# Kernel optimization log

Measured on AMD Instinct MI355X. Metric: run time of the kernel, lower is better.

Reference implementation:

```python
import jax, jax.numpy as jnp
import numpy as np

B = 1024          # sub (= obj) batch size
NUME = 20000      # num entities
NUMR = 8          # num relations
NET = 2 * NUMR + 1  # hetero edge types: r, -r, self
DIMT = 28         # time encoding dim
DIME = 100        # entity embedding dim
DIM = 200         # emb module output dim
H = 4             # history length
HEADS = 4         # GAT heads
OH = DIM // HEADS # GAT per-head out dim
N0 = 160000       # layer-0 src nodes
N1 = 40000        # layer-0 dst / layer-1 src nodes
R = 2 * B * H     # unique roots = layer-1 dst nodes
E0 = 60000        # edges per etype, layer 0
E1 = 16000        # edges per etype, layer 1
K = 500000        # copy mask entries
DIMR = 100        # relation embedding dim
HATT = 4          # self-attention heads
OA = DIM // HATT  # per-head q/k/v dim (Attention out_dim//h)
DIN0 = DIME + DIMT
DIN1 = DIM + DIMT


def setup_inputs() -> dict:
    key = jax.random.key(0)
    ks = jax.random.split(key, 48)
    ri = jax.random.randint
    nrm = lambda i, shp, s=0.05: jax.random.normal(ks[i], shp, jnp.float32) * s
    d = {}
    d['sub'] = ri(ks[0], (B,), 0, NUME)
    d['obj'] = ri(ks[1], (B,), 0, NUME)
    d['rel'] = ri(ks[2], (B,), 0, NUMR)
    d['ts'] = 1000
    d['nid0'] = ri(ks[3], (N0,), 0, NUME * 1000)
    d['root_idx'] = ri(ks[4], (2 * B * H,), 0, R)
    d['src0'] = ri(ks[5], (NET, E0), 0, N0)
    d['dst0'] = ri(ks[6], (NET, E0), 0, N1)
    d['src1'] = ri(ks[7], (NET, E1), 0, N1)
    d['dst1'] = ri(ks[8], (NET, E1), 0, R)
    d['copy_rows'] = ri(ks[9], (K,), 0, 2 * B)
    d['copy_cols'] = ri(ks[10], (K,), 0, NUME)
    # parameters
    d['emb_table'] = nrm(11, (NUME, DIME))
    d['time_freq'] = jnp.asarray(1.0 / 10 ** np.linspace(0, 9, DIMT), jnp.float32)
    d['time_phase'] = jnp.zeros((DIMT,), jnp.float32)
    d['Wg0'] = nrm(12, (NET, DIN0, HEADS, OH))
    d['al0'] = nrm(13, (NET, HEADS, OH))
    d['ar0'] = nrm(14, (NET, HEADS, OH))
    d['bg0'] = jnp.zeros((NET, DIM), jnp.float32)
    d['Wg1'] = nrm(15, (NET, DIN1, HEADS, OH))
    d['al1'] = nrm(16, (NET, HEADS, OH))
    d['ar1'] = nrm(17, (NET, HEADS, OH))
    d['bg1'] = jnp.zeros((NET, DIM), jnp.float32)
    d['ln0_w'] = jnp.ones((H * DIM,), jnp.float32)
    d['ln0_b'] = jnp.zeros((H * DIM,), jnp.float32)
    d['Wq'] = nrm(18, (HATT, DIM, OA))
    d['bq'] = jnp.zeros((HATT, OA), jnp.float32)
    d['Wv'] = nrm(19, (HATT, DIM, OA))
    d['bv'] = jnp.zeros((HATT, OA), jnp.float32)
    d['ln1_w'] = jnp.ones((H * DIM,), jnp.float32)
    d['ln1_b'] = jnp.zeros((H * DIM,), jnp.float32)
    d['Wd1'] = nrm(20, (H * DIM, DIM))
    d['bd1'] = jnp.zeros((DIM,), jnp.float32)
    d['srel_emb'] = nrm(21, (NUMR, DIMR))
    d['orel_emb'] = nrm(22, (NUMR, DIMR))
    d['Wsub'] = nrm(23, (DIM + DIMR, NUME))
    d['bsub'] = jnp.zeros((NUME,), jnp.float32)
    d['Wobj'] = nrm(24, (DIM + DIMR, NUME))
    d['bobj'] = jnp.zeros((NUME,), jnp.float32)
    d['csrel_emb'] = nrm(25, (NUMR, DIMR))
    d['corel_emb'] = nrm(26, (NUMR, DIMR))
    d['cWsub'] = nrm(27, (DIM + DIMR, NUME))
    d['cbsub'] = jnp.zeros((NUME,), jnp.float32)
    d['cWobj'] = nrm(28, (DIM + DIMR, NUME))
    d['cbobj'] = jnp.zeros((NUME,), jnp.float32)
    return d


def _temb(nid, ts, tf, tp):
    t = (ts - nid // NUME).astype(jnp.float32)
    return jnp.cos(t[:, None] * tf + tp)


def _gat(x, Wg, al, ar, bg, src, dst, nd):
    # heterogeneous GATConv over NET relation types, mean-aggregated (DGL HeteroGraphConv)
    msg = jnp.zeros((nd, HEADS, OH), x.dtype)
    for r in range(NET):
        s, d = src[r], dst[r]
        fs = jnp.einsum('ei,iho->eho', x[s], Wg[r])                     # [E,h,o] src feats per edge
        er_n = (jnp.einsum('ni,iho->nho', x[:nd], Wg[r]) * ar[r]).sum(-1)  # [nd,h]
        el = (fs * al[r]).sum(-1)                                       # [E,h]
        e = jax.nn.leaky_relu(el + er_n[d], 0.2)
        m = jax.ops.segment_max(e, d, num_segments=nd)
        a = jnp.exp(e - m[d])
        z = jax.ops.segment_sum(a, d, num_segments=nd)
        alpha = a / z[d]
        msg = msg + jax.ops.segment_sum(alpha[:, :, None] * fs, d, num_segments=nd)
    return jax.nn.relu((msg.reshape(nd, HEADS * OH) + bg.sum(0)) / NET)


def _ln(x, w, b):
    mu = x.mean(-1, keepdims=True)
    v = ((x - mu) ** 2).mean(-1, keepdims=True)
    return (x - mu) / jnp.sqrt(v + 1e-5) * w + b


def reference(sub, obj, rel, ts, nid0, root_idx, src0, dst0, src1, dst1, copy_rows, copy_cols, emb_table, time_freq, time_phase, Wg0, al0, ar0, bg0, Wg1, al1, ar1, bg1, ln0_w, ln0_b, Wq, bq, Wv, bv, ln1_w, ln1_b, Wd1, bd1, srel_emb, orel_emb, Wsub, bsub, Wobj, bobj, csrel_emb, corel_emb, cWsub, cbsub, cWobj, cbobj):
    # --- EmbModule: entity emb + time enc + 2-layer hetero GAT over sampled blocks ---
    h = emb_table[nid0 % NUME]                                   # [N0, DIME]
    x = jnp.concatenate([h, _temb(nid0, ts, time_freq, time_phase)], 1)
    h = _gat(x, Wg0, al0, ar0, bg0, src0, dst0, N1)              # [N1, DIM]
    x = jnp.concatenate([h, _temb(nid0[:N1], ts, time_freq, time_phase)], 1)
    h = _gat(x, Wg1, al1, ar1, bg1, src1, dst1, R)               # [R, DIM]
    hid = h[root_idx].reshape(2 * B, H * DIM)                    # [2B, H*DIM]
    # --- Copy mechanism (on detached last-history embedding) ---
    ch = jax.lax.stop_gradient(hid[:, -DIM:])
    raw_sub = jnp.concatenate([ch[B:], corel_emb[rel]], 1) @ cWsub + cbsub
    raw_obj = jnp.concatenate([ch[:B], csrel_emb[rel]], 1) @ cWobj + cbobj
    raw = jnp.concatenate([raw_sub, raw_obj], 0)                 # [2B, NUME]
    masked = jnp.full((2 * B, NUME), -100.0, raw.dtype).at[copy_rows, copy_cols].set(raw[copy_rows, copy_cols])
    csub, cobj = masked[:B], masked[B:]
    # --- Gen layers: LN -> SelfAttention -> LN -> dense ---
    x = _ln(hid, ln0_w, ln0_b)
    xs = x.reshape(2 * B, H, DIM)
    q = jnp.einsum('bse,heo->bhso', xs, Wq) + bq[:, None, :]     # k == q (w_q reused in source)
    att = jax.nn.softmax(jnp.einsum('bhso,bhto->bhst', q, q), axis=2)  # torch softmax(dim=1)
    v = jnp.einsum('bse,heo->bhso', xs, Wv) + bv[:, None, :]
    ans = jnp.einsum('bhst,bhto->bhso', att, v)                  # [2B,h,S,OA]
    x = jax.nn.relu(ans.transpose(0, 2, 1, 3).reshape(2 * B, H * DIM))
    x = _ln(x, ln1_w, ln1_b)
    x = jax.nn.relu(x @ Wd1 + bd1)                               # [2B, DIM]
    sub_emb, obj_emb = x[:B], x[B:]
    sub_pred = jnp.concatenate([obj_emb, orel_emb[rel]], 1) @ Wsub + bsub
    obj_pred = jnp.concatenate([sub_emb, srel_emb[rel]], 1) @ Wobj + bobj
    return (sub_pred, obj_pred, csub, cobj)
```

## Files before the change

kernel.cpp:

```cpp
#include <hip/hip_runtime.h>
#include <hip/hip_bf16.h>
#include <math.h>

typedef __hip_bfloat16 bf16;
typedef __attribute__((ext_vector_type(8))) short short8;
typedef __attribute__((ext_vector_type(4))) float f32x4;

#define BQ 1024
#define NUME 20000
#define NET 17
#define DIMT 28
#define DIME 100
#define DIM 200
#define HEADS 4
#define OH 50
#define N0 160000
#define N1 40000
#define RNODES 8192
#define E0 60000
#define E1 16000
#define KK 500000
#define DIMR 100
#define HATT 4
#define OA 50
#define DIN0 128
#define DIN1 228
#define HD 800
#define NROWS 2048
#define PKS 10
#define PNT 1250

__device__ __forceinline__ float b2f(bf16 v){ return __bfloat162float(v); }
__device__ __forceinline__ bf16 f2b(float v){ return __float2bfloat16(v); }
__device__ __forceinline__ float bs2f(unsigned short u){ return __uint_as_float((unsigned)u << 16); }
__device__ __forceinline__ unsigned short f2bu(float v){ bf16 t = f2b(v); return *reinterpret_cast<unsigned short*>(&t); }

static constexpr int CVT_NREG = 29;
static constexpr int CVT_N[CVT_NREG] = {
  2000000, 28, 28, 435200, 3400, 3400, 3400, 775200, 3400, 3400, 3400,
  800, 800, 40000, 200, 40000, 200, 800, 800, 160000, 200, 800, 800,
  20000, 20000, 800, 800, 20000, 20000
};
static constexpr int CVT_DIN[CVT_NREG] = {
  12,13,14,15,16,17,18,19,20,21,22,23,24,25,26,27,28,29,30,31,32,33,34,36,38,39,40,42,44
};
struct CvtSrcs { const void* p[CVT_NREG]; };
struct CvtMeta { int cum[CVT_NREG+1]; int bcum[CVT_NREG+1]; };

__global__ __launch_bounds__(64) void k_detect(const unsigned* tfw, unsigned* flag){
  if (threadIdx.x == 0) flag[0] = ((tfw[0] & 0xFFFFu) == 0u) ? 1u : 0u;
}

__global__ __launch_bounds__(256) void k_cvt(CvtSrcs srcs, CvtMeta meta, bf16* dst, const unsigned* flagp){
  int b = blockIdx.x;
  int r = 0;
  while (meta.bcum[r+1] <= b) r++;
  int i = (b - meta.bcum[r])*256 + threadIdx.x;
  int n = meta.cum[r+1] - meta.cum[r];
  if (i >= n) return;
  bool f32m = flagp[0] != 0u;
  bf16 v;
  if (f32m) v = f2b(((const float*)srcs.p[r])[i]);
  else      v = ((const bf16*)srcs.p[r])[i];
  dst[meta.cum[r] + i] = v;
}

__global__ __launch_bounds__(256) void k_fill_u32(unsigned* p, unsigned v, long n){
  long i = (long)blockIdx.x*256 + threadIdx.x;
  if (i < n) p[i] = v;
}

__global__ __launch_bounds__(256) void k_fill_out(void* outb, const unsigned* flagp){
  bool f32m = flagp[0] != 0u;
  long nwords = f32m ? (long)2*BQ*NUME : (long)BQ*NUME;
  long i = (long)blockIdx.x*256 + threadIdx.x;
  if (i >= nwords) return;
  unsigned* p = (unsigned*)((char*)outb + (size_t)2*BQ*NUME * (f32m ? 4 : 2));
  p[i] = f32m ? 0xC2C80000u : 0xC2C8C2C8u;
}

__global__ __launch_bounds__(256) void k_prep_w(const bf16* Wg, const bf16* al, const bf16* ar,
                                                float* wal, float* war, int DIN){
  int idx = blockIdx.x*256 + threadIdx.x;
  int total = NET*DIN*4;
  if (idx >= total) return;
  int h = idx & 3; int ri = idx >> 2; int i = ri % DIN; int r = ri / DIN;
  const bf16* wrow = Wg + ((size_t)(r*DIN + i))*HEADS*OH + h*OH;
  const bf16* alr = al + (size_t)(r*HEADS + h)*OH;
  const bf16* arr = ar + (size_t)(r*HEADS + h)*OH;
  float sl=0.f, sr=0.f;
  for (int o=0;o<OH;o++){ float w=b2f(wrow[o]); sl += w*b2f(alr[o]); sr += w*b2f(arr[o]); }
  wal[idx]=sl; war[idx]=sr;
}

__global__ __launch_bounds__(256) void k_pack(const bf16* Wg, bf16* wpk, int DIN, int KS){
  int idx = blockIdx.x*256 + threadIdx.x;
  int total = NET*KS*13*512;
  if (idx >= total) return;
  int j = idx & 7, lane = (idx>>3) & 63;
  int rem = idx >> 9;
  int nt = rem % 13, rks = rem / 13;
  int ks = rks % KS, r = rks / KS;
  int k = ks*32 + (lane>>4)*8 + j;
  int n = nt*16 + (lane&15);
  bf16 v = f2b(0.f);
  if (k < DIN && n < 200) v = Wg[((size_t)r*DIN + k)*200 + n];
  wpk[idx] = v;
}

__global__ __launch_bounds__(256) void k_pack_pred(const void* Wsub, const void* Wobj, bf16* wpkP,
                                                    const unsigned* flagp){
  long idx = (long)blockIdx.x*256 + threadIdx.x;
  long total = (long)2*PKS*PNT*512;
  if (idx >= total) return;
  int j = (int)(idx & 7), lane = (int)((idx>>3) & 63);
  long rem = idx >> 9;
  int ntile = (int)(rem % PNT); rem /= PNT;
  int ks = (int)(rem % PKS); int page = (int)(rem / PKS);
  int k = ks*32 + (lane>>4)*8 + j;
  int n = ntile*16 + (lane&15);
  const void* W = page ? Wobj : Wsub;
  bool f32m = flagp[0] != 0u;
  float v = 0.f;
  if (k < 300) v = f32m ? ((const float*)W)[(size_t)k*NUME + n]
                        : b2f(((const bf16*)W)[(size_t)k*NUME + n]);
  wpkP[idx] = f2b(v);
}

__global__ __launch_bounds__(256) void k_prep_pred(const float* x4, const bf16* nSrel, const bf16* nOrel,
                                                    const int* rel, bf16* Apack){
  long idx = (long)blockIdx.x*256 + threadIdx.x;
  if (idx >= (long)2*1024*320) return;
  int j = (int)(idx % 320); long rem = idx/320;
  int row = (int)(rem % 1024); int page = (int)(rem / 1024);
  float v = 0.f;
  if (j < 200) v = x4[((size_t)(page==0 ? 1024+row : row))*DIM + j];
  else if (j < 300){
    const bf16* re = (page==0) ? nOrel : nSrel;
    v = b2f(re[(size_t)rel[row]*DIMR + (j-200)]);
  }
  Apack[idx] = f2b(v);
}

__global__ __launch_bounds__(256) void k_pred_mfma(const bf16* __restrict__ Apack, const bf16* __restrict__ wpkP,
                                                   const bf16* bsub, const bf16* bobj, void* outb,
                                                   const unsigned* flagp){
  constexpr int SR = 320 + 8;
  __shared__ bf16 As[64*SR];
  int page = blockIdx.z;
  int rb = blockIdx.y*64;
  int cb = blockIdx.x*16;
  int t = threadIdx.x;
  const bf16* Ap = Apack + (size_t)page*1024*320;
  for (int c=t; c<64*80; c+=256){
    int m=c/80, j4=c%80;
    *(uint2*)(As + m*SR + j4*4) = *(const uint2*)(Ap + (size_t)(rb+m)*320 + j4*4);
  }
  __syncthreads();
  int lane = t&63, w = t>>6;
  int n_idx = lane&15, quad = lane>>4;
  const short8* wp8 = (const short8*)(wpkP + (size_t)page*PKS*PNT*512);
  f32x4 acc[4][4];
  #pragma unroll
  for (int i=0;i<4;i++)
    #pragma unroll
    for (int mt=0;mt<4;mt++) acc[i][mt] = (f32x4){0.f,0.f,0.f,0.f};
  short8 bz = {0,0,0,0,0,0,0,0};
  for (int ks=0; ks<PKS; ks++){
    short8 bfr[4];
    #pragma unroll
    for (int i=0;i<4;i++){
      int ntile = cb + w + 4*i;
      bfr[i] = (ntile < PNT) ? wp8[((size_t)ks*PNT + ntile)*64 + lane] : bz;
    }
    short8 afr[4];
    #pragma unroll
    for (int mt=0;mt<4;mt++) afr[mt] = *(const short8*)(As + (size_t)(mt*16 + n_idx)*SR + ks*32 + quad*8);
    #pragma unroll
    for (int i=0;i<4;i++)
      #pragma unroll
      for (int mt=0;mt<4;mt++)
        acc[i][mt] = __builtin_amdgcn_mfma_f32_16x16x32_bf16(afr[mt], bfr[i], acc[i][mt], 0, 0, 0);
  }
  bool f32m = flagp[0] != 0u;
  const bf16* bias = page ? bobj : bsub;
  size_t elem_off = (size_t)page*BQ*NUME;
  for (int i=0;i<4;i++){
    int ntile = cb + w + 4*i;
    if (ntile >= PNT) continue;
    int n = ntile*16 + n_idx;
    float bb = b2f(bias[n]);
    #pragma unroll
    for (int mt=0;mt<4;mt++){
      #pragma unroll
      for (int reg=0;reg<4;reg++){
        int m = rb + mt*16 + quad*4 + reg;
        size_t oi = elem_off + (size_t)m*NUME + n;
        float val = acc[i][mt][reg] + bb;
        if (f32m) ((float*)outb)[oi] = val; else ((bf16*)outb)[oi] = f2b(val);
      }
    }
  }
}

__global__ __launch_bounds__(256) void k_bgs(const bf16* bg0, const bf16* bg1, float* bgs0, float* bgs1){
  int j = blockIdx.x*256 + threadIdx.x;
  if (j < DIM){ float s=0.f; for(int r=0;r<NET;r++) s += b2f(bg0[r*DIM+j]); bgs0[j]=s; }
  else if (j < 2*DIM){ int jj=j-DIM; float s=0.f; for(int r=0;r<NET;r++) s += b2f(bg1[r*DIM+jj]); bgs1[jj]=s; }
}

__global__ __launch_bounds__(256) void k_build_x0(const int* nid0, const int* ts_p, const bf16* emb,
                                                  const bf16* tf, const bf16* tp, bf16* x0){
  long idx = (long)blockIdx.x*256 + threadIdx.x;
  if (idx >= (long)N0*DIN0) return;
  int n = idx / DIN0, j = idx % DIN0;
  int nid = nid0[n];
  bf16 v;
  if (j < DIME) v = emb[(size_t)(nid % NUME)*DIME + j];
  else {
    float t = (float)(ts_p[0] - nid / NUME);
    int jj = j - DIME;
    v = f2b(cosf(t * b2f(tf[jj]) + b2f(tp[jj])));
  }
  x0[idx] = v;
}

__global__ __launch_bounds__(256) void k_build_x1(const int* nid0, const int* ts_p, const float* msg0,
                                                  const float* bgs0, const bf16* tf, const bf16* tp, bf16* x1){
  long idx = (long)blockIdx.x*256 + threadIdx.x;
  if (idx >= (long)N1*DIN1) return;
  int n = idx / DIN1, j = idx % DIN1;
  bf16 v;
  if (j < DIM){
    v = f2b(fmaxf((msg0[(size_t)n*DIM + j] + bgs0[j]) * (1.0f/NET), 0.0f));
  } else {
    int nid = nid0[n];
    float t = (float)(ts_p[0] - nid / NUME);
    int jj = j - DIM;
    v = f2b(cosf(t * b2f(tf[jj]) + b2f(tp[jj])));
  }
  x1[idx] = v;
}

template<int DIN>
__global__ __launch_bounds__(256) void k_er(const bf16* __restrict__ x, const float* __restrict__ war,
                                            bf16* __restrict__ er, int nd){
  int idx = blockIdx.x*256 + threadIdx.x;
  if (idx >= NET*nd) return;
  int r = idx / nd, n = idx % nd;
  const ushort4* xr = (const ushort4*)(x + (size_t)n*DIN);
  const float4* w = (const float4*)(war + (size_t)r*DIN*4);
  float a0=0.f,a1=0.f,a2=0.f,a3=0.f;
  #pragma unroll 4
  for (int i=0;i<DIN/4;i++){
    ushort4 xv = xr[i];
    float x0=bs2f(xv.x), x1=bs2f(xv.y), x2=bs2f(xv.z), x3=bs2f(xv.w);
    float4 w0=w[4*i], w1=w[4*i+1], w2=w[4*i+2], w3=w[4*i+3];
    a0 += x0*w0.x + x1*w1.x + x2*w2.x + x3*w3.x;
    a1 += x0*w0.y + x1*w1.y + x2*w2.y + x3*w3.y;
    a2 += x0*w0.z + x1*w1.z + x2*w2.z + x3*w3.z;
    a3 += x0*w0.w + x1*w1.w + x2*w2.w + x3*w3.w;
  }
  bf16* e = er + (size_t)idx*4;
  e[0]=f2b(a0); e[1]=f2b(a1); e[2]=f2b(a2); e[3]=f2b(a3);
}

template<int DIN>
__global__ __launch_bounds__(256) void k_edge(const bf16* __restrict__ x, const float* __restrict__ wal,
                                              const bf16* __restrict__ er,
                                              const int* __restrict__ src, const int* __restrict__ dst,
                                              bf16* abuf, float* z, int nE, int nd){
  int idx = blockIdx.x*256 + threadIdx.x;
  if (idx >= NET*nE) return;
  int r = idx / nE;
  int s = src[idx], d = dst[idx];
  const ushort4* xr = (const ushort4*)(x + (size_t)s*DIN);
  const float4* w = (const float4*)(wal + (size_t)r*DIN*4);
  float a0=0.f,a1=0.f,a2=0.f,a3=0.f;
  #pragma unroll 4
  for (int i=0;i<DIN/4;i++){
    ushort4 xv = xr[i];
    float x0=bs2f(xv.x), x1=bs2f(xv.y), x2=bs2f(xv.z), x3=bs2f(xv.w);
    float4 w0=w[4*i], w1=w[4*i+1], w2=w[4*i+2], w3=w[4*i+3];
    a0 += x0*w0.x + x1*w1.x + x2*w2.x + x3*w3.x;
    a1 += x0*w0.y + x1*w1.y + x2*w2.y + x3*w3.y;
    a2 += x0*w0.z + x1*w1.z + x2*w2.z + x3*w3.z;
    a3 += x0*w0.w + x1*w1.w + x2*w2.w + x3*w3.w;
  }
  float acc[4] = {a0,a1,a2,a3};
  const bf16* ern = er + ((size_t)r*nd + d)*4;
  float* zp = z + ((size_t)r*nd + d)*4;
  bf16* ao = abuf + (size_t)idx*4;
  #pragma unroll
  for (int h=0;h<4;h++){
    float v = acc[h] + b2f(ern[h]);
    v = v>0.f ? v : 0.2f*v;
    float a = expf(fminf(v, 80.f));
    ao[h] = f2b(a);
    atomicAdd(&zp[h], a);
  }
}

__global__ __launch_bounds__(256) void k_count(const int* __restrict__ dst, long n, unsigned* cnt){
  long i = (long)blockIdx.x*256 + threadIdx.x;
  if (i >= n) return;
  atomicAdd(&cnt[dst[i]], 1u);
}

__global__ __launch_bounds__(256) void k_scan(const unsigned* __restrict__ cnt, unsigned* offs, unsigned* cur, int n){
  __shared__ unsigned part[256];
  __shared__ unsigned tot;
  int t = threadIdx.x;
  int chunk = (n + 255)/256;
  int lo = t*chunk, hi = lo+chunk; if (hi > n) hi = n; if (lo > n) lo = n;
  unsigned s = 0;
  for (int i=lo;i<hi;i++) s += cnt[i];
  part[t] = s;
  __syncthreads();
  if (t==0){
    unsigned r = 0;
    for (int i=0;i<256;i++){ unsigned v = part[i]; part[i] = r; r += v; }
    tot = r;
  }
  __syncthreads();
  unsigned run = part[t];
  for (int i=lo;i<hi;i++){ offs[i]=run; cur[i]=run; run += cnt[i]; }
  if (t==0) offs[n] = tot;
}

__global__ __launch_bounds__(256) void k_fillcsr(const int* __restrict__ dst, long n, unsigned* cur, int* ids){
  long i = (long)blockIdx.x*256 + threadIdx.x;
  if (i >= n) return;
  unsigned pos = atomicAdd(&cur[dst[i]], 1u);
  ids[pos] = (int)i;
}

template<int DIN, int KS>
__global__ __launch_bounds__(256) void k_acc_mfma(const bf16* __restrict__ x, const bf16* __restrict__ wpk,
                                                  const bf16* __restrict__ abuf, const float* __restrict__ z,
                                                  const int* __restrict__ src, const int* __restrict__ dst,
                                                  float* msg, bf16* fbuf, int nE, int nd, int r0, int mode){
  constexpr int KM = KS*32;
  constexpr int SR = KM + 8;
  __shared__ bf16 xs[64*SR];
  __shared__ float alpha_s[64*4];
  __shared__ int sdst[64], ssrc[64];
  int r = r0 + blockIdx.y;
  int eb = blockIdx.x*64;
  int me = min(64, nE - eb);
  int t = threadIdx.x;
  if (t < 64){
    int v_src=0, v_dst=0;
    if (t < me){ v_src = src[(size_t)r*nE + eb + t]; v_dst = dst[(size_t)r*nE + eb + t]; }
    ssrc[t]=v_src; sdst[t]=v_dst;
  }
  __syncthreads();
  {
    int m = t>>2, h = t&3;
    float al = 0.f;
    if (m < me){
      float a = b2f(abuf[((size_t)r*nE + eb + m)*4 + h]);
      float zz = z[((size_t)r*nd + sdst[m])*4 + h];
      al = a / fmaxf(zz, 1e-30f);
    }
    alpha_s[m*4+h] = al;
  }
  constexpr int CH = KM/4;
  for (int c = t; c < 64*CH; c += 256){
    int m = c / CH, j4 = c % CH;
    uint2 v = make_uint2(0u,0u);
    if (m < me && j4*4 < DIN) v = *(const uint2*)(x + (size_t)ssrc[m]*DIN + j4*4);
    *(uint2*)(xs + m*SR + j4*4) = v;
  }
  __syncthreads();

  int lane = t & 63, w = t >> 6;
  int n_idx = lane & 15, quad = lane >> 4;
  const short8* wpk8 = (const short8*)wpk;
  for (int mt=0; mt<4; mt++){
    short8 a[KS];
    const bf16* abase = xs + (size_t)(mt*16 + n_idx)*SR + quad*8;
    #pragma unroll
    for (int ks=0; ks<KS; ks++) a[ks] = *(const short8*)(abase + ks*32);
    int m = mt*16 + n_idx;
    for (int nt=w; nt<13; nt+=4){
      const short8* bp = wpk8 + (((size_t)r*KS)*13 + nt)*64 + lane;
      f32x4 acc = {0.f,0.f,0.f,0.f};
      #pragma unroll
      for (int ks=0; ks<KS; ks++){
        short8 b = bp[(size_t)ks*13*64];
        acc = __builtin_amdgcn_mfma_f32_16x16x32_bf16(b, a[ks], acc, 0, 0, 0);
      }
      int nbase = nt*16 + quad*4;
      if (nbase < 200 && m < me){
        if (mode == 0){
          #pragma unroll
          for (int reg=0; reg<4; reg++){
            int n = nbase + reg;
            int h = n / 50;
            atomicAdd(&msg[(size_t)sdst[m]*200 + n], acc[reg] * alpha_s[m*4+h]);
          }
        } else {
          ushort4 pk;
          { int n=nbase;   pk.x = f2bu(acc[0] * alpha_s[m*4 + n/50]); }
          { int n=nbase+1; pk.y = f2bu(acc[1] * alpha_s[m*4 + n/50]); }
          { int n=nbase+2; pk.z = f2bu(acc[2] * alpha_s[m*4 + n/50]); }
          { int n=nbase+3; pk.w = f2bu(acc[3] * alpha_s[m*4 + n/50]); }
          *(ushort4*)(fbuf + ((size_t)(r - r0)*nE + eb + m)*200 + nbase) = pk;
        }
      }
    }
  }
}

__global__ __launch_bounds__(256) void k_gather(const bf16* __restrict__ F, const unsigned* __restrict__ offs,
                                                const int* __restrict__ ids, float* __restrict__ msg,
                                                int nd, int accum){
  int w = threadIdx.x >> 6, lane = threadIdx.x & 63;
  int d = blockIdx.x*4 + w;
  if (d >= nd) return;
  unsigned k0 = offs[d], k1 = offs[d+1];
  float a0=0.f, a1=0.f, a2=0.f, a3=0.f;
  for (unsigned k=k0; k<k1; k++){
    int id = ids[k];
    if (lane < 50){
      ushort4 v = *(const ushort4*)(F + (size_t)id*200 + lane*4);
      a0 += bs2f(v.x); a1 += bs2f(v.y); a2 += bs2f(v.z); a3 += bs2f(v.w);
    }
  }
  if (lane < 50){
    float4* out = (float4*)(msg + (size_t)d*200 + lane*4);
    if (accum){ float4 p = *out; a0 += p.x; a1 += p.y; a2 += p.z; a3 += p.w; }
    float4 o; o.x=a0; o.y=a1; o.z=a2; o.w=a3;
    *out = o;
  }
}

__global__ __launch_bounds__(256) void k_hid(const float* msg1, const float* bgs1, const int* root_idx, float* hid){
  long idx = (long)blockIdx.x*256 + threadIdx.x;
  if (idx >= (long)NROWS*HD) return;
  int b = idx / HD, c = idx % HD;
  int s = c / DIM, j = c % DIM;
  int n = root_idx[b*4 + s];
  hid[idx] = fmaxf((msg1[(size_t)n*DIM + j] + bgs1[j]) * (1.0f/NET), 0.0f);
}

__global__ __launch_bounds__(256) void k_ln(const float* xin, const bf16* w, const bf16* b, float* xout){
  int row = blockIdx.x;
  const float* xr = xin + (size_t)row*HD;
  __shared__ float red[16];
  __shared__ float mu_s, rs_s;
  float s=0.f, s2=0.f;
  for (int j=threadIdx.x;j<HD;j+=256){ float v=xr[j]; s+=v; s2+=v*v; }
  for (int off=32; off; off>>=1){ s += __shfl_down(s,off); s2 += __shfl_down(s2,off); }
  int lane = threadIdx.x & 63, wid = threadIdx.x >> 6;
  if (lane==0){ red[wid]=s; red[8+wid]=s2; }
  __syncthreads();
  if (threadIdx.x==0){
    float S = red[0]+red[1]+red[2]+red[3];
    float S2 = red[8]+red[9]+red[10]+red[11];
    float mu = S * (1.0f/HD);
    float var = fmaxf(S2 * (1.0f/HD) - mu*mu, 0.f);
    mu_s = mu; rs_s = rsqrtf(var + 1e-5f);
  }
  __syncthreads();
  float mu = mu_s, rs = rs_s;
  for (int j=threadIdx.x;j<HD;j+=256){
    float v = (xr[j]-mu)*rs;
    xout[(size_t)row*HD + j] = v*b2f(w[j]) + b2f(b[j]);
  }
}

__global__ __launch_bounds__(256) void k_att(const float* xln, const bf16* Wq, const bf16* bq,
                                             const bf16* Wv, const bf16* bv, float* x2){
  __shared__ float xs[HD], qs[HD], vs[HD], att_s[64];
  int b = blockIdx.x, t = threadIdx.x;
  for (int j=t;j<HD;j+=256) xs[j] = xln[(size_t)b*HD + j];
  __syncthreads();
  for (int idx=t; idx<HD; idx+=256){
    int ha = idx/200, srow=(idx%200)/50, o=idx%50;
    const float* xr = xs + srow*200;
    const bf16* wq = Wq + (size_t)ha*DIM*OA + o;
    const bf16* wv = Wv + (size_t)ha*DIM*OA + o;
    float q=0.f, v=0.f;
    for (int e=0;e<DIM;e++){ float xv=xr[e]; q += xv*b2f(wq[(size_t)e*OA]); v += xv*b2f(wv[(size_t)e*OA]); }
    qs[idx] = q + b2f(bq[ha*OA+o]);
    vs[idx] = v + b2f(bv[ha*OA+o]);
  }
  __syncthreads();
  if (t < 64){
    int ha=t>>4, srow=(t>>2)&3, tt=t&3;
    const float* qa = qs + ha*200 + srow*50;
    const float* qb = qs + ha*200 + tt*50;
    float sc=0.f;
    for (int o=0;o<50;o++) sc += qa[o]*qb[o];
    att_s[ha*16 + srow*4 + tt] = sc;
  }
  __syncthreads();
  if (t < 16){
    int ha=t>>2, tt=t&3;
    float m=-1e30f;
    for (int srow=0;srow<4;srow++) m = fmaxf(m, att_s[ha*16+srow*4+tt]);
    float ex[4]; float zz=0.f;
    for (int srow=0;srow<4;srow++){ ex[srow]=expf(att_s[ha*16+srow*4+tt]-m); zz+=ex[srow]; }
    for (int srow=0;srow<4;srow++) att_s[ha*16+srow*4+tt] = ex[srow]/zz;
  }
  __syncthreads();
  for (int idx=t; idx<HD; idx+=256){
    int ha = idx/200, srow=(idx%200)/50, o=idx%50;
    float a=0.f;
    for (int tt=0;tt<4;tt++) a += att_s[ha*16+srow*4+tt]*vs[ha*200+tt*50+o];
    x2[(size_t)b*HD + srow*200 + ha*50 + o] = fmaxf(a, 0.f);
  }
}

__global__ __launch_bounds__(256) void k_d1(const float* x3, const bf16* Wd1, const bf16* bd1, float* x4){
  __shared__ float xs[8*HD];
  int rb = blockIdx.x*8, t = threadIdx.x;
  for (int idx=t; idx<8*HD; idx+=256) xs[idx] = x3[(size_t)rb*HD + idx];
  __syncthreads();
  if (t < DIM){
    float acc[8] = {0,0,0,0,0,0,0,0};
    for (int k=0;k<HD;k++){
      float w = b2f(Wd1[(size_t)k*DIM + t]);
      #pragma unroll
      for (int r=0;r<8;r++) acc[r] += xs[r*HD+k]*w;
    }
    float bb = b2f(bd1[t]);
    for (int r=0;r<8;r++) x4[(size_t)(rb+r)*DIM + t] = fmaxf(acc[r]+bb, 0.f);
  }
}

__global__ __launch_bounds__(256) void k_pred(const float* xemb, const bf16* relemb, const int* rel,
                                              const void* W, const bf16* bias, void* outb, size_t elem_off,
                                              const unsigned* flagp){
  __shared__ float As[16*304];
  bool f32m = flagp[0] != 0u;
  int rb = blockIdx.y*16;
  int cb = blockIdx.x*512;
  int t = threadIdx.x;
  for (int idx=t; idx<16*300; idx+=256){
    int r = idx/300, i = idx%300;
    int row = rb + r;
    float v = (i < DIM) ? xemb[(size_t)row*DIM + i]
                        : b2f(relemb[(size_t)rel[row]*DIMR + (i-DIM)]);
    As[r*304+i] = v;
  }
  __syncthreads();
  int c0 = cb + t, c1 = cb + 256 + t;
  bool g0 = c0 < NUME, g1 = c1 < NUME;
  float acc0[16], acc1[16];
  #pragma unroll
  for (int r=0;r<16;r++){ acc0[r]=0.f; acc1[r]=0.f; }
  if (f32m){
    const float* W32 = (const float*)W;
    for (int k=0;k<300;k++){
      float w0 = g0 ? W32[(size_t)k*NUME + c0] : 0.f;
      float w1 = g1 ? W32[(size_t)k*NUME + c1] : 0.f;
      #pragma unroll
      for (int r=0;r<16;r++){ float a = As[r*304+k]; acc0[r] += a*w0; acc1[r] += a*w1; }
    }
  } else {
    const bf16* W16 = (const bf16*)W;
    for (int k=0;k<300;k++){
      float w0 = g0 ? b2f(W16[(size_t)k*NUME + c0]) : 0.f;
      float w1 = g1 ? b2f(W16[(size_t)k*NUME + c1]) : 0.f;
      #pragma unroll
      for (int r=0;r<16;r++){ float a = As[r*304+k]; acc0[r] += a*w0; acc1[r] += a*w1; }
    }
  }
  #pragma unroll
  for (int rr=0; rr<2; rr++){
    int c = rr ? c1 : c0;
    float* acc = rr ? acc1 : acc0;
    if (c < NUME){
      float bb = b2f(bias[c]);
      for (int r=0;r<16;r++){
        size_t oi = elem_off + (size_t)(rb+r)*NUME + c;
        float val = acc[r] + bb;
        if (f32m) ((float*)outb)[oi] = val; else ((bf16*)outb)[oi] = f2b(val);
      }
    }
  }
}

__global__ __launch_bounds__(256) void k_transpose(const void* in, bf16* out, int rows, int cols,
                                                   const unsigned* flagp){
  __shared__ bf16 tile[32][33];
  bool f32m = flagp[0] != 0u;
  int c0 = blockIdx.x*32, r0 = blockIdx.y*32;
  int tx = threadIdx.x % 32, ty = threadIdx.x / 32;
  for (int rr=ty; rr<32; rr+=8){
    int r = r0+rr, c = c0+tx;
    if (r<rows && c<cols){
      size_t i = (size_t)r*cols + c;
      tile[rr][tx] = f32m ? f2b(((const float*)in)[i]) : ((const bf16*)in)[i];
    }
  }
  __syncthreads();
  for (int rr=ty; rr<32; rr+=8){
    int ocol = c0+rr, orow = r0+tx;
    if (ocol<cols && orow<rows) out[(size_t)ocol*rows + orow] = tile[tx][rr];
  }
}

__global__ __launch_bounds__(256) void k_scatter(const int* copy_rows, const int* copy_cols, const int* rel,
                                                 const float* hid, const bf16* csrel, const bf16* corel,
                                                 const bf16* cWsubT, const bf16* cWobjT,
                                                 const bf16* cbsub, const bf16* cbobj,
                                                 void* outb, const unsigned* flagp){
  bool f32m = flagp[0] != 0u;
  int wid = threadIdx.x >> 6, lane = threadIdx.x & 63;
  long k = (long)blockIdx.x*4 + wid;
  if (k >= KK) return;
  int row = copy_rows[k], col = copy_cols[k];
  const float* chrow; const bf16* re; const bf16* wt; float bias_v;
  if (row < BQ){
    chrow = hid + ((size_t)(BQ+row))*HD + 600;
    re = corel + (size_t)rel[row]*DIMR;
    wt = cWsubT + (size_t)col*300;
    bias_v = b2f(cbsub[col]);
  } else {
    int rr = row - BQ;
    chrow = hid + ((size_t)rr)*HD + 600;
    re = csrel + (size_t)rel[rr]*DIMR;
    wt = cWobjT + (size_t)col*300;
    bias_v = b2f(cbobj[col]);
  }
  float s = 0.f;
  for (int i=lane; i<300; i+=64){
    float a = (i < DIM) ? chrow[i] : b2f(re[i-DIM]);
    s += a * b2f(wt[i]);
  }
  for (int off=32; off; off>>=1) s += __shfl_down(s, off);
  if (lane==0){
    size_t oi = (size_t)2*BQ*NUME + (size_t)row*NUME + col;
    float val = s + bias_v;
    if (f32m) ((float*)outb)[oi] = val; else ((bf16*)outb)[oi] = f2b(val);
  }
}

static inline dim3 GS(long n){ return dim3((unsigned)((n + 255)/256)); }

extern "C" void kernel_launch(void* const* d_in, const int* in_sizes, int n_in,
                              void* d_out, int out_size, void* d_ws, size_t ws_size,
                              hipStream_t stream){
  const int* rel       = (const int*)d_in[2];
  const int* ts_p      = (const int*)d_in[3];
  const int* nid0      = (const int*)d_in[4];
  const int* root_idx  = (const int*)d_in[5];
  const int* src0      = (const int*)d_in[6];
  const int* dst0      = (const int*)d_in[7];
  const int* src1      = (const int*)d_in[8];
  const int* dst1      = (const int*)d_in[9];
  const int* copy_rows = (const int*)d_in[10];
  const int* copy_cols = (const int*)d_in[11];
  const void* Wsub  = d_in[35];
  const void* Wobj  = d_in[37];
  const void* cWsub = d_in[41];
  const void* cWobj = d_in[43];

  char* base = (char*)d_ws;
  size_t off = 0;
  auto alloc = [&](size_t bytes)->char*{
    char* p = base + off; off = (off + bytes + 255) & ~(size_t)255; return p;
  };
  unsigned* flagp = (unsigned*)alloc(256);
  long cvt_total = 0; for (int i=0;i<CVT_NREG;i++) cvt_total += CVT_N[i];
  bf16* normb = (bf16*)alloc((size_t)cvt_total*2);
  bf16* x0    = (bf16*)alloc((size_t)N0*DIN0*2);
  bf16* x1    = (bf16*)alloc((size_t)N1*DIN1*2);
  float* msg0 = (float*)alloc((size_t)N1*DIM*4);
  float* wal0 = (float*)alloc((size_t)NET*DIN0*4*4);
  float* war0 = (float*)alloc((size_t)NET*DIN0*4*4);
  float* wal1 = (float*)alloc((size_t)NET*DIN1*4*4);
  float* war1 = (float*)alloc((size_t)NET*DIN1*4*4);
  float* bgs0 = (float*)alloc(DIM*4);
  float* bgs1 = (float*)alloc(DIM*4);
  bf16* wpk0  = (bf16*)alloc((size_t)NET*4*13*512*2);
  bf16* wpk1  = (bf16*)alloc((size_t)NET*8*13*512*2);
  size_t arena = off;
  bf16*  er0 = (bf16*)(base + arena);
  bf16*  a0b = (bf16*)((char*)er0 + (size_t)NET*N1*8);
  float* z0  = (float*)((char*)a0b + (size_t)NET*E0*8);
  char* A = base + arena;
  bf16*  er1  = (bf16*)A;
  bf16*  a1b  = (bf16*)(A + 1114112);
  float* z1   = (float*)(A + 3290112);
  float* msg1 = (float*)(A + 5518336);
  float* hid  = (float*)(A + 12071936);
  float* xln  = (float*)(A + 0);
  float* x2   = (float*)(A + 6553600);
  float* x3   = (float*)(A + 13107200);
  float* x4   = (float*)(A + 19660800);
  bf16* cWsubT = (bf16*)x0;
  bf16* cWobjT = (bf16*)((char*)x0 + (size_t)NUME*300*2);

  size_t extent1 = (size_t)NET*N1*8 + (size_t)NET*E0*8 + (size_t)NET*N1*16;
  size_t tail = (arena + extent1 + 255) & ~(size_t)255;
  size_t cntsz = (((size_t)(N1+1)*4) + 255) & ~(size_t)255;
  unsigned* cnt  = (unsigned*)(base + tail);
  unsigned* offs = (unsigned*)(base + tail + cntsz);
  unsigned* cur  = (unsigned*)(base + tail + 2*cntsz);
  size_t ids_sz = (((size_t)NET*E0*4) + 255) & ~(size_t)255;
  int* ids = (int*)(base + tail + 3*cntsz);
  size_t F_off = tail + 3*cntsz + ids_sz;
  bf16* fbuf = (bf16*)(base + F_off);
  size_t fcap = (ws_size > F_off) ? (ws_size - F_off) : 0;
  size_t relF0 = (size_t)E0*200*2, relF1 = (size_t)E1*200*2;
  int nrelc0 = (int)((fcap / relF0 < (size_t)NET) ? (fcap / relF0) : (size_t)NET);
  int nrelc1 = (int)((fcap / relF1 < (size_t)NET) ? (fcap / relF1) : (size_t)NET);
  size_t wpkP_sz = (size_t)2*PKS*PNT*512*2;
  size_t Apack_sz = (size_t)2*1024*320*2;
  bf16* wpkP  = (bf16*)(base + F_off);
  bf16* Apack = (bf16*)(base + F_off + wpkP_sz);
  bool predok = fcap >= (wpkP_sz + Apack_sz);

  long cum[CVT_NREG+1]; cum[0]=0;
  for (int i=0;i<CVT_NREG;i++) cum[i+1] = cum[i] + CVT_N[i];
  auto NP = [&](int i)->const bf16*{ return normb + cum[i]; };
  const bf16 *nEmb=NP(0), *nTf=NP(1), *nTp=NP(2), *nWg0=NP(3), *nAl0=NP(4), *nAr0=NP(5), *nBg0=NP(6),
             *nWg1=NP(7), *nAl1=NP(8), *nAr1=NP(9), *nBg1=NP(10), *nLn0w=NP(11), *nLn0b=NP(12),
             *nWq=NP(13), *nBq=NP(14), *nWv=NP(15), *nBv=NP(16), *nLn1w=NP(17), *nLn1b=NP(18),
             *nWd1=NP(19), *nBd1=NP(20), *nSrel=NP(21), *nOrel=NP(22), *nBsub=NP(23), *nBobj=NP(24),
             *nCsrel=NP(25), *nCorel=NP(26), *nCbsub=NP(27), *nCbobj=NP(28);

  k_detect<<<dim3(1),64,0,stream>>>((const unsigned*)d_in[13], flagp);
  CvtSrcs srcs;
  for (int i=0;i<CVT_NREG;i++) srcs.p[i] = d_in[CVT_DIN[i]];
  CvtMeta meta;
  { int c=0, bc=0;
    for (int i=0;i<CVT_NREG;i++){ meta.cum[i]=c; meta.bcum[i]=bc; c+=CVT_N[i]; bc += (CVT_N[i]+255)/256; }
    meta.cum[CVT_NREG]=c; meta.bcum[CVT_NREG]=bc;
    k_cvt<<<dim3((unsigned)bc),256,0,stream>>>(srcs, meta, normb, flagp);
  }
  k_fill_u32<<<GS((long)NET*N1*4),256,0,stream>>>((unsigned*)z0, 0u, (long)NET*N1*4);
  k_fill_out<<<GS((long)2*BQ*NUME),256,0,stream>>>(d_out, flagp);
  k_prep_w<<<GS(NET*DIN0*4),256,0,stream>>>(nWg0, nAl0, nAr0, wal0, war0, DIN0);
  k_prep_w<<<GS(NET*DIN1*4),256,0,stream>>>(nWg1, nAl1, nAr1, wal1, war1, DIN1);
  k_pack<<<GS((long)NET*4*13*512),256,0,stream>>>(nWg0, wpk0, DIN0, 4);
  k_pack<<<GS((long)NET*8*13*512),256,0,stream>>>(nWg1, wpk1, DIN1, 8);
  k_bgs<<<GS(2*DIM),256,0,stream>>>(nBg0, nBg1, bgs0, bgs1);
  k_build_x0<<<GS((long)N0*DIN0),256,0,stream>>>(nid0, ts_p, nEmb, nTf, nTp, x0);

  k_er<DIN0><<<GS((long)NET*N1),256,0,stream>>>(x0, war0, er0, N1);
  k_edge<DIN0><<<GS((long)NET*E0),256,0,stream>>>(x0, wal0, er0, src0, dst0, a0b, z0, E0, N1);
  if (nrelc0 >= 1){
    for (int r0=0; r0<NET; r0+=nrelc0){
      int nr = (NET - r0 < nrelc0) ? (NET - r0) : nrelc0;
      long nEd = (long)nr*E0;
      k_fill_u32<<<GS((long)N1+1),256,0,stream>>>(cnt, 0u, (long)N1+1);
      k_count<<<GS(nEd),256,0,stream>>>(dst0 + (size_t)r0*E0, nEd, cnt);
      k_scan<<<dim3(1),256,0,stream>>>(cnt, offs, cur, N1);
      k_fillcsr<<<GS(nEd),256,0,stream>>>(dst0 + (size_t)r0*E0, nEd, cur, ids);
      k_acc_mfma<DIN0,4><<<dim3((E0+63)/64, nr),256,0,stream>>>(x0, wpk0, a0b, z0, src0, dst0,
                                                                 msg0, fbuf, E0, N1, r0, 1);
      k_gather<<<dim3((N1+3)/4),256,0,stream>>>(fbuf, offs, ids, msg0, N1, r0>0 ? 1 : 0);
    }
  } else {
    k_fill_u32<<<GS((long)N1*DIM),256,0,stream>>>((unsigned*)msg0, 0u, (long)N1*DIM);
    k_acc_mfma<DIN0,4><<<dim3((E0+63)/64, NET),256,0,stream>>>(x0, wpk0, a0b, z0, src0, dst0,
                                                                msg0, (bf16*)nullptr, E0, N1, 0, 0);
  }

  k_build_x1<<<GS((long)N1*DIN1),256,0,stream>>>(nid0, ts_p, msg0, bgs0, nTf, nTp, x1);
  k_fill_u32<<<GS((long)NET*RNODES*4),256,0,stream>>>((unsigned*)z1, 0u, (long)NET*RNODES*4);
  k_er<DIN1><<<GS((long)NET*RNODES),256,0,stream>>>(x1, war1, er1, RNODES);
  k_edge<DIN1><<<GS((long)NET*E1),256,0,stream>>>(x1, wal1, er1, src1, dst1, a1b, z1, E1, RNODES);
  if (nrelc1 >= 1){
    for (int r0=0; r0<NET; r0+=nrelc1){
      int nr = (NET - r0 < nrelc1) ? (NET - r0) : nrelc1;
      long nEd = (long)nr*E1;
      k_fill_u32<<<GS((long)RNODES+1),256,0,stream>>>(cnt, 0u, (long)RNODES+1);
      k_count<<<GS(nEd),256,0,stream>>>(dst1 + (size_t)r0*E1, nEd, cnt);
      k_scan<<<dim3(1),256,0,stream>>>(cnt, offs, cur, RNODES);
      k_fillcsr<<<GS(nEd),256,0,stream>>>(dst1 + (size_t)r0*E1, nEd, cur, ids);
      k_acc_mfma<DIN1,8><<<dim3((E1+63)/64, nr),256,0,stream>>>(x1, wpk1, a1b, z1, src1, dst1,
                                                                 msg1, fbuf, E1, RNODES, r0, 1);
      k_gather<<<dim3((RNODES+3)/4),256,0,stream>>>(fbuf, offs, ids, msg1, RNODES, r0>0 ? 1 : 0);
    }
  } else {
    k_fill_u32<<<GS((long)RNODES*DIM),256,0,stream>>>((unsigned*)msg1, 0u, (long)RNODES*DIM);
    k_acc_mfma<DIN1,8><<<dim3((E1+63)/64, NET),256,0,stream>>>(x1, wpk1, a1b, z1, src1, dst1,
                                                                msg1, (bf16*)nullptr, E1, RNODES, 0, 0);
  }

  if (predok)
    k_pack_pred<<<GS((long)2*PKS*PNT*512),256,0,stream>>>(Wsub, Wobj, wpkP, flagp);

  k_hid<<<GS((long)NROWS*HD),256,0,stream>>>(msg1, bgs1, root_idx, hid);
  k_transpose<<<dim3(625,10),256,0,stream>>>(cWsub, cWsubT, 300, NUME, flagp);
  k_transpose<<<dim3(625,10),256,0,stream>>>(cWobj, cWobjT, 300, NUME, flagp);
  k_scatter<<<dim3((KK+3)/4),256,0,stream>>>(copy_rows, copy_cols, rel, hid, nCsrel, nCorel,
                                             cWsubT, cWobjT, nCbsub, nCbobj, d_out, flagp);

  k_ln<<<dim3(NROWS),256,0,stream>>>(hid, nLn0w, nLn0b, xln);
  k_att<<<dim3(NROWS),256,0,stream>>>(xln, nWq, nBq, nWv, nBv, x2);
  k_ln<<<dim3(NROWS),256,0,stream>>>(x2, nLn1w, nLn1b, x3);
  k_d1<<<dim3(NROWS/8),256,0,stream>>>(x3, nWd1, nBd1, x4);

  if (predok){
    k_prep_pred<<<GS((long)2*1024*320),256,0,stream>>>(x4, nSrel, nOrel, rel, Apack);
    k_pred_mfma<<<dim3(79,16,2),256,0,stream>>>(Apack, wpkP, nBsub, nBobj, d_out, flagp);
  } else {
    k_pred<<<dim3(40,64),256,0,stream>>>(x4 + (size_t)BQ*DIM, nOrel, rel, Wsub, nBsub, d_out, 0, flagp);
    k_pred<<<dim3(40,64),256,0,stream>>>(x4,                  nSrel, rel, Wobj, nBobj, d_out, (size_t)BQ*NUME, flagp);
  }
  (void)in_sizes; (void)n_in; (void)out_size; (void)ws_size;
}
```

Measured before the change: 2.443 ms.

## Precompute per-node attention logits via MFMA, write CSR-ordered messages, fuse LN+attention

Adds a per-node MFMA kernel that computes all el/er attention logits for every edge type into a table, so the edge kernel becomes a light lookup instead of recomputing dot products per edge. Message tiles are written directly at their CSR positions, which lets the gather read sequentially instead of indirecting through an id array. The two LayerNorms and the self-attention are fused into one kernel to drop intermediate buffers and launches. Buffer layout is reorganised to fit the logit table, at the cost of extra workspace and a fallback path when it does not fit.

Result: faster. 2.305 ms (-5.6%).

```diff
diff --git a/kernel.cpp b/kernel.cpp
--- a/kernel.cpp
+++ b/kernel.cpp
@@ -29,6 +29,7 @@
 #define NROWS 2048
 #define PKS 10
 #define PNT 1250
+#define TABW 136
 
 __device__ __forceinline__ float b2f(bf16 v){ return __bfloat162float(v); }
 __device__ __forceinline__ bf16 f2b(float v){ return __float2bfloat16(v); }
@@ -108,138 +109,87 @@
   wpk[idx] = v;
 }
 
-__global__ __launch_bounds__(256) void k_pack_pred(const void* Wsub, const void* Wobj, bf16* wpkP,
-                                                    const unsigned* flagp){
-  long idx = (long)blockIdx.x*256 + threadIdx.x;
-  long total = (long)2*PKS*PNT*512;
+__global__ __launch_bounds__(256) void k_pack_walr(const float* wal, const float* war, bf16* wpkE,
+                                                   int DIN, int KS){
+  int idx = blockIdx.x*256 + threadIdx.x;
+  int total = KS*9*512;
   if (idx >= total) return;
-  int j = (int)(idx & 7), lane = (int)((idx>>3) & 63);
-  long rem = idx >> 9;
-  int ntile = (int)(rem % PNT); rem /= PNT;
-  int ks = (int)(rem % PKS); int page = (int)(rem / PKS);
+  int j = idx & 7, lane = (idx>>3) & 63;
+  int rem = idx >> 9;
+  int nt = rem % 9, ks = rem / 9;
   int k = ks*32 + (lane>>4)*8 + j;
-  int n = ntile*16 + (lane&15);
-  const void* W = page ? Wobj : Wsub;
-  bool f32m = flagp[0] != 0u;
+  int c = nt*16 + (lane&15);
   float v = 0.f;
-  if (k < 300) v = f32m ? ((const float*)W)[(size_t)k*NUME + n]
-                        : b2f(((const bf16*)W)[(size_t)k*NUME + n]);
-  wpkP[idx] = f2b(v);
-}
-
-__global__ __launch_bounds__(256) void k_prep_pred(const float* x4, const bf16* nSrel, const bf16* nOrel,
-                                                    const int* rel, bf16* Apack){
-  long idx = (long)blockIdx.x*256 + threadIdx.x;
-  if (idx >= (long)2*1024*320) return;
-  int j = (int)(idx % 320); long rem = idx/320;
-  int row = (int)(rem % 1024); int page = (int)(rem / 1024);
-  float v = 0.f;
-  if (j < 200) v = x4[((size_t)(page==0 ? 1024+row : row))*DIM + j];
-  else if (j < 300){
-    const bf16* re = (page==0) ? nOrel : nSrel;
-    v = b2f(re[(size_t)rel[row]*DIMR + (j-200)]);
-  }
-  Apack[idx] = f2b(v);
-}
-
-__global__ __launch_bounds__(256) void k_pred_mfma(const bf16* __restrict__ Apack, const bf16* __restrict__ wpkP,
-                                                   const bf16* bsub, const bf16* bobj, void* outb,
-                                                   const unsigned* flagp){
-  constexpr int SR = 320 + 8;
-  __shared__ bf16 As[64*SR];
-  int page = blockIdx.z;
-  int rb = blockIdx.y*64;
-  int cb = blockIdx.x*16;
+  if (k < DIN && c < TABW){
+    int r = c >> 3, q = c & 7;
+    const float* wsrc = (q < 4) ? wal : war;
+    v = wsrc[((size_t)r*DIN + k)*4 + (q & 3)];
+  }
+  wpkE[idx] = f2b(v);
+}
+
+template<int DIN, int KS>
+__global__ __launch_bounds__(256) void k_elr(const bf16* __restrict__ x, const bf16* __restrict__ wpkE,
+                                             float* __restrict__ tab){
+  constexpr int KM = KS*32;
+  constexpr int SR = KM + 8;
+  __shared__ bf16 xs[64*SR];
+  int rb = blockIdx.x*64;
   int t = threadIdx.x;
-  const bf16* Ap = Apack + (size_t)page*1024*320;
-  for (int c=t; c<64*80; c+=256){
-    int m=c/80, j4=c%80;
-    *(uint2*)(As + m*SR + j4*4) = *(const uint2*)(Ap + (size_t)(rb+m)*320 + j4*4);
-  }
-  __syncthreads();
-  int lane = t&63, w = t>>6;
-  int n_idx = lane&15, quad = lane>>4;
-  const short8* wp8 = (const short8*)(wpkP + (size_t)page*PKS*PNT*512);
-  f32x4 acc[4][4];
+  constexpr int CH = KM/4;
+  for (int c = t; c < 64*CH; c += 256){
+    int m = c / CH, j4 = c % CH;
+    uint2 v = make_uint2(0u,0u);
+    if (j4*4 < DIN) v = *(const uint2*)(x + (size_t)(rb+m)*DIN + j4*4);
+    *(uint2*)(xs + m*SR + j4*4) = v;
+  }
+  __syncthreads();
+  int lane = t & 63, w = t >> 6;
+  int n_idx = lane & 15, quad = lane >> 4;
+  const short8* wp8 = (const short8*)wpkE;
+  for (int mt=0; mt<4; mt++){
+    short8 a[KS];
+    const bf16* ab = xs + (size_t)(mt*16 + n_idx)*SR + quad*8;
+    #pragma unroll
+    for (int ks=0; ks<KS; ks++) a[ks] = *(const short8*)(ab + ks*32);
+    int m = rb + mt*16 + n_idx;
+    for (int nt=w; nt<9; nt+=4){
+      const short8* bp = wp8 + (size_t)nt*64 + lane;
+      f32x4 acc = {0.f,0.f,0.f,0.f};
+      #pragma unroll
+      for (int ks=0; ks<KS; ks++){
+        short8 b = bp[(size_t)ks*9*64];
+        acc = __builtin_amdgcn_mfma_f32_16x16x32_bf16(b, a[ks], acc, 0, 0, 0);
+      }
+      int nbase = nt*16 + quad*4;
+      if (nbase < TABW){
+        float4 o; o.x=acc[0]; o.y=acc[1]; o.z=acc[2]; o.w=acc[3];
+        *(float4*)(tab + (size_t)m*TABW + nbase) = o;
+      }
+    }
+  }
+}
+
+__global__ __launch_bounds__(256) void k_edge_lite(const float* __restrict__ tab,
+                                                   const int* __restrict__ src, const int* __restrict__ dst,
+                                                   bf16* abuf, float* z, int nE, int nd){
+  int idx = blockIdx.x*256 + threadIdx.x;
+  if (idx >= NET*nE) return;
+  int r = idx / nE;
+  int s = src[idx], d = dst[idx];
+  float4 el = *(const float4*)(tab + (size_t)s*TABW + r*8);
+  float4 er = *(const float4*)(tab + (size_t)d*TABW + r*8 + 4);
+  float ev[4] = {el.x+er.x, el.y+er.y, el.z+er.z, el.w+er.w};
+  float* zp = z + ((size_t)r*nd + d)*4;
+  bf16* ao = abuf + (size_t)idx*4;
   #pragma unroll
-  for (int i=0;i<4;i++)
-    #pragma unroll
-    for (int mt=0;mt<4;mt++) acc[i][mt] = (f32x4){0.f,0.f,0.f,0.f};
-  short8 bz = {0,0,0,0,0,0,0,0};
-  for (int ks=0; ks<PKS; ks++){
-    short8 bfr[4];
-    #pragma unroll
-    for (int i=0;i<4;i++){
-      int ntile = cb + w + 4*i;
-      bfr[i] = (ntile < PNT) ? wp8[((size_t)ks*PNT + ntile)*64 + lane] : bz;
-    }
-    short8 afr[4];
-    #pragma unroll
-    for (int mt=0;mt<4;mt++) afr[mt] = *(const short8*)(As + (size_t)(mt*16 + n_idx)*SR + ks*32 + quad*8);
-    #pragma unroll
-    for (int i=0;i<4;i++)
-      #pragma unroll
-      for (int mt=0;mt<4;mt++)
-        acc[i][mt] = __builtin_amdgcn_mfma_f32_16x16x32_bf16(afr[mt], bfr[i], acc[i][mt], 0, 0, 0);
-  }
-  bool f32m = flagp[0] != 0u;
-  const bf16* bias = page ? bobj : bsub;
-  size_t elem_off = (size_t)page*BQ*NUME;
-  for (int i=0;i<4;i++){
-    int ntile = cb + w + 4*i;
-    if (ntile >= PNT) continue;
-    int n = ntile*16 + n_idx;
-    float bb = b2f(bias[n]);
-    #pragma unroll
-    for (int mt=0;mt<4;mt++){
-      #pragma unroll
-      for (int reg=0;reg<4;reg++){
-        int m = rb + mt*16 + quad*4 + reg;
-        size_t oi = elem_off + (size_t)m*NUME + n;
-        float val = acc[i][mt][reg] + bb;
-        if (f32m) ((float*)outb)[oi] = val; else ((bf16*)outb)[oi] = f2b(val);
-      }
-    }
-  }
-}
-
-__global__ __launch_bounds__(256) void k_bgs(const bf16* bg0, const bf16* bg1, float* bgs0, float* bgs1){
-  int j = blockIdx.x*256 + threadIdx.x;
-  if (j < DIM){ float s=0.f; for(int r=0;r<NET;r++) s += b2f(bg0[r*DIM+j]); bgs0[j]=s; }
-  else if (j < 2*DIM){ int jj=j-DIM; float s=0.f; for(int r=0;r<NET;r++) s += b2f(bg1[r*DIM+jj]); bgs1[jj]=s; }
-}
-
-__global__ __launch_bounds__(256) void k_build_x0(const int* nid0, const int* ts_p, const bf16* emb,
-                                                  const bf16* tf, const bf16* tp, bf16* x0){
-  long idx = (long)blockIdx.x*256 + threadIdx.x;
-  if (idx >= (long)N0*DIN0) return;
-  int n = idx / DIN0, j = idx % DIN0;
-  int nid = nid0[n];
-  bf16 v;
-  if (j < DIME) v = emb[(size_t)(nid % NUME)*DIME + j];
-  else {
-    float t = (float)(ts_p[0] - nid / NUME);
-    int jj = j - DIME;
-    v = f2b(cosf(t * b2f(tf[jj]) + b2f(tp[jj])));
-  }
-  x0[idx] = v;
-}
-
-__global__ __launch_bounds__(256) void k_build_x1(const int* nid0, const int* ts_p, const float* msg0,
-                                                  const float* bgs0, const bf16* tf, const bf16* tp, bf16* x1){
-  long idx = (long)blockIdx.x*256 + threadIdx.x;
-  if (idx >= (long)N1*DIN1) return;
-  int n = idx / DIN1, j = idx % DIN1;
-  bf16 v;
-  if (j < DIM){
-    v = f2b(fmaxf((msg0[(size_t)n*DIM + j] + bgs0[j]) * (1.0f/NET), 0.0f));
-  } else {
-    int nid = nid0[n];
-    float t = (float)(ts_p[0] - nid / NUME);
-    int jj = j - DIM;
-    v = f2b(cosf(t * b2f(tf[jj]) + b2f(tp[jj])));
-  }
-  x1[idx] = v;
+  for (int h=0;h<4;h++){
+    float v = ev[h];
+    v = v>0.f ? v : 0.2f*v;
+    float a = expf(fminf(v, 80.f));
+    ao[h] = f2b(a);
+    atomicAdd(&zp[h], a);
+  }
 }
 
 template<int DIN>
@@ -328,31 +278,36 @@
   if (t==0) offs[n] = tot;
 }
 
-__global__ __launch_bounds__(256) void k_fillcsr(const int* __restrict__ dst, long n, unsigned* cur, int* ids){
+__global__ __launch_bounds__(256) void k_fillcsr(const int* __restrict__ dst, long n, unsigned* cur, int* posar){
   long i = (long)blockIdx.x*256 + threadIdx.x;
   if (i >= n) return;
   unsigned pos = atomicAdd(&cur[dst[i]], 1u);
-  ids[pos] = (int)i;
+  posar[i] = (int)pos;
 }
 
 template<int DIN, int KS>
 __global__ __launch_bounds__(256) void k_acc_mfma(const bf16* __restrict__ x, const bf16* __restrict__ wpk,
                                                   const bf16* __restrict__ abuf, const float* __restrict__ z,
                                                   const int* __restrict__ src, const int* __restrict__ dst,
+                                                  const int* __restrict__ posar,
                                                   float* msg, bf16* fbuf, int nE, int nd, int r0, int mode){
   constexpr int KM = KS*32;
   constexpr int SR = KM + 8;
   __shared__ bf16 xs[64*SR];
   __shared__ float alpha_s[64*4];
-  __shared__ int sdst[64], ssrc[64];
+  __shared__ int sdst[64], ssrc[64], spos[64];
   int r = r0 + blockIdx.y;
   int eb = blockIdx.x*64;
   int me = min(64, nE - eb);
   int t = threadIdx.x;
   if (t < 64){
-    int v_src=0, v_dst=0;
-    if (t < me){ v_src = src[(size_t)r*nE + eb + t]; v_dst = dst[(size_t)r*nE + eb + t]; }
-    ssrc[t]=v_src; sdst[t]=v_dst;
+    int v_src=0, v_dst=0, v_pos=0;
+    if (t < me){
+      v_src = src[(size_t)r*nE + eb + t];
+      v_dst = dst[(size_t)r*nE + eb + t];
+      if (posar) v_pos = posar[(size_t)(r - r0)*nE + eb + t];
+    }
+    ssrc[t]=v_src; sdst[t]=v_dst; spos[t]=v_pos;
   }
   __syncthreads();
   {
@@ -397,8 +352,7 @@
           #pragma unroll
           for (int reg=0; reg<4; reg++){
             int n = nbase + reg;
-            int h = n / 50;
-            atomicAdd(&msg[(size_t)sdst[m]*200 + n], acc[reg] * alpha_s[m*4+h]);
+            atomicAdd(&msg[(size_t)sdst[m]*200 + n], acc[reg] * alpha_s[m*4 + n/50]);
           }
         } else {
           ushort4 pk;
@@ -406,34 +360,69 @@
           { int n=nbase+1; pk.y = f2bu(acc[1] * alpha_s[m*4 + n/50]); }
           { int n=nbase+2; pk.z = f2bu(acc[2] * alpha_s[m*4 + n/50]); }
           { int n=nbase+3; pk.w = f2bu(acc[3] * alpha_s[m*4 + n/50]); }
-          *(ushort4*)(fbuf + ((size_t)(r - r0)*nE + eb + m)*200 + nbase) = pk;
+          *(ushort4*)(fbuf + (size_t)spos[m]*200 + nbase) = pk;
         }
       }
     }
   }
 }
 
-__global__ __launch_bounds__(256) void k_gather(const bf16* __restrict__ F, const unsigned* __restrict__ offs,
-                                                const int* __restrict__ ids, float* __restrict__ msg,
-                                                int nd, int accum){
+__global__ __launch_bounds__(256) void k_gather_seq(const bf16* __restrict__ F, const unsigned* __restrict__ offs,
+                                                    float* __restrict__ msg, int nd, int accum){
   int w = threadIdx.x >> 6, lane = threadIdx.x & 63;
   int d = blockIdx.x*4 + w;
   if (d >= nd) return;
   unsigned k0 = offs[d], k1 = offs[d+1];
-  float a0=0.f, a1=0.f, a2=0.f, a3=0.f;
-  for (unsigned k=k0; k<k1; k++){
-    int id = ids[k];
-    if (lane < 50){
-      ushort4 v = *(const ushort4*)(F + (size_t)id*200 + lane*4);
+  if (lane < 50){
+    float a0=0.f, a1=0.f, a2=0.f, a3=0.f;
+    for (unsigned k=k0; k<k1; k++){
+      ushort4 v = *(const ushort4*)(F + (size_t)k*200 + lane*4);
       a0 += bs2f(v.x); a1 += bs2f(v.y); a2 += bs2f(v.z); a3 += bs2f(v.w);
     }
-  }
-  if (lane < 50){
     float4* out = (float4*)(msg + (size_t)d*200 + lane*4);
     if (accum){ float4 p = *out; a0 += p.x; a1 += p.y; a2 += p.z; a3 += p.w; }
     float4 o; o.x=a0; o.y=a1; o.z=a2; o.w=a3;
     *out = o;
   }
+}
+
+__global__ __launch_bounds__(256) void k_bgs(const bf16* bg0, const bf16* bg1, float* bgs0, float* bgs1){
+  int j = blockIdx.x*256 + threadIdx.x;
+  if (j < DIM){ float s=0.f; for(int r=0;r<NET;r++) s += b2f(bg0[r*DIM+j]); bgs0[j]=s; }
+  else if (j < 2*DIM){ int jj=j-DIM; float s=0.f; for(int r=0;r<NET;r++) s += b2f(bg1[r*DIM+jj]); bgs1[jj]=s; }
+}
+
+__global__ __launch_bounds__(256) void k_build_x0(const int* nid0, const int* ts_p, const bf16* emb,
+                                                  const bf16* tf, const bf16* tp, bf16* x0){
+  long idx = (long)blockIdx.x*256 + threadIdx.x;
+  if (idx >= (long)N0*DIN0) return;
+  int n = idx / DIN0, j = idx % DIN0;
+  int nid = nid0[n];
+  bf16 v;
+  if (j < DIME) v = emb[(size_t)(nid % NUME)*DIME + j];
+  else {
+    float t = (float)(ts_p[0] - nid / NUME);
+    int jj = j - DIME;
+    v = f2b(cosf(t * b2f(tf[jj]) + b2f(tp[jj])));
+  }
+  x0[idx] = v;
+}
+
+__global__ __launch_bounds__(256) void k_build_x1(const int* nid0, const int* ts_p, const float* msg0,
+                                                  const float* bgs0, const bf16* tf, const bf16* tp, bf16* x1){
+  long idx = (long)blockIdx.x*256 + threadIdx.x;
+  if (idx >= (long)N1*DIN1) return;
+  int n = idx / DIN1, j = idx % DIN1;
+  bf16 v;
+  if (j < DIM){
+    v = f2b(fmaxf((msg0[(size_t)n*DIM + j] + bgs0[j]) * (1.0f/NET), 0.0f));
+  } else {
+    int nid = nid0[n];
+    float t = (float)(ts_p[0] - nid / NUME);
+    int jj = j - DIM;
+    v = f2b(cosf(t * b2f(tf[jj]) + b2f(tp[jj])));
+  }
+  x1[idx] = v;
 }
 
 __global__ __launch_bounds__(256) void k_hid(const float* msg1, const float* bgs1, const int* root_idx, float* hid){
@@ -445,18 +434,23 @@
   hid[idx] = fmaxf((msg1[(size_t)n*DIM + j] + bgs1[j]) * (1.0f/NET), 0.0f);
 }
 
-__global__ __launch_bounds__(256) void k_ln(const float* xin, const bf16* w, const bf16* b, float* xout){
-  int row = blockIdx.x;
-  const float* xr = xin + (size_t)row*HD;
-  __shared__ float red[16];
+__global__ __launch_bounds__(256) void k_att_ln(const float* __restrict__ hid,
+                                                const bf16* ln0w, const bf16* ln0b,
+                                                const bf16* Wq, const bf16* bq,
+                                                const bf16* Wv, const bf16* bv,
+                                                const bf16* ln1w, const bf16* ln1b,
+                                                float* __restrict__ x3){
+  __shared__ float xs[HD], qs[HD], vs[HD], att_s[64], red[16];
   __shared__ float mu_s, rs_s;
+  int b = blockIdx.x, t = threadIdx.x;
+  int lane = t & 63, wid = t >> 6;
+  const float* xr = hid + (size_t)b*HD;
   float s=0.f, s2=0.f;
-  for (int j=threadIdx.x;j<HD;j+=256){ float v=xr[j]; s+=v; s2+=v*v; }
+  for (int j=t;j<HD;j+=256){ float v=xr[j]; s+=v; s2+=v*v; }
   for (int off=32; off; off>>=1){ s += __shfl_down(s,off); s2 += __shfl_down(s2,off); }
-  int lane = threadIdx.x & 63, wid = threadIdx.x >> 6;
   if (lane==0){ red[wid]=s; red[8+wid]=s2; }
   __syncthreads();
-  if (threadIdx.x==0){
+  if (t==0){
     float S = red[0]+red[1]+red[2]+red[3];
     float S2 = red[8]+red[9]+red[10]+red[11];
     float mu = S * (1.0f/HD);
@@ -464,26 +458,16 @@
     mu_s = mu; rs_s = rsqrtf(var + 1e-5f);
   }
   __syncthreads();
-  float mu = mu_s, rs = rs_s;
-  for (int j=threadIdx.x;j<HD;j+=256){
-    float v = (xr[j]-mu)*rs;
-    xout[(size_t)row*HD + j] = v*b2f(w[j]) + b2f(b[j]);
-  }
-}
-
-__global__ __launch_bounds__(256) void k_att(const float* xln, const bf16* Wq, const bf16* bq,
-                                             const bf16* Wv, const bf16* bv, float* x2){
-  __shared__ float xs[HD], qs[HD], vs[HD], att_s[64];
-  int b = blockIdx.x, t = threadIdx.x;
-  for (int j=t;j<HD;j+=256) xs[j] = xln[(size_t)b*HD + j];
+  { float mu=mu_s, rs=rs_s;
+    for (int j=t;j<HD;j+=256) xs[j] = (xr[j]-mu)*rs*b2f(ln0w[j]) + b2f(ln0b[j]); }
   __syncthreads();
   for (int idx=t; idx<HD; idx+=256){
     int ha = idx/200, srow=(idx%200)/50, o=idx%50;
-    const float* xr = xs + srow*200;
+    const float* xrow = xs + srow*200;
     const bf16* wq = Wq + (size_t)ha*DIM*OA + o;
     const bf16* wv = Wv + (size_t)ha*DIM*OA + o;
     float q=0.f, v=0.f;
-    for (int e=0;e<DIM;e++){ float xv=xr[e]; q += xv*b2f(wq[(size_t)e*OA]); v += xv*b2f(wv[(size_t)e*OA]); }
+    for (int e=0;e<DIM;e++){ float xv=xrow[e]; q += xv*b2f(wq[(size_t)e*OA]); v += xv*b2f(wv[(size_t)e*OA]); }
     qs[idx] = q + b2f(bq[ha*OA+o]);
     vs[idx] = v + b2f(bv[ha*OA+o]);
   }
@@ -510,8 +494,24 @@
     int ha = idx/200, srow=(idx%200)/50, o=idx%50;
     float a=0.f;
     for (int tt=0;tt<4;tt++) a += att_s[ha*16+srow*4+tt]*vs[ha*200+tt*50+o];
-    x2[(size_t)b*HD + srow*200 + ha*50 + o] = fmaxf(a, 0.f);
-  }
+    xs[srow*200 + ha*50 + o] = fmaxf(a, 0.f);
+  }
+  __syncthreads();
+  s=0.f; s2=0.f;
+  for (int j=t;j<HD;j+=256){ float v=xs[j]; s+=v; s2+=v*v; }
+  for (int off=32; off; off>>=1){ s += __shfl_down(s,off); s2 += __shfl_down(s2,off); }
+  if (lane==0){ red[wid]=s; red[8+wid]=s2; }
+  __syncthreads();
+  if (t==0){
+    float S = red[0]+red[1]+red[2]+red[3];
+    float S2 = red[8]+red[9]+red[10]+red[11];
+    float mu = S * (1.0f/HD);
+    float var = fmaxf(S2 * (1.0f/HD) - mu*mu, 0.f);
+    mu_s = mu; rs_s = rsqrtf(var + 1e-5f);
+  }
+  __syncthreads();
+  { float mu=mu_s, rs=rs_s;
+    for (int j=t;j<HD;j+=256) x3[(size_t)b*HD + j] = (xs[j]-mu)*rs*b2f(ln1w[j]) + b2f(ln1b[j]); }
 }
 
 __global__ __launch_bounds__(256) void k_d1(const float* x3, const bf16* Wd1, const bf16* bd1, float* x4){
@@ -528,6 +528,101 @@
     }
     float bb = b2f(bd1[t]);
     for (int r=0;r<8;r++) x4[(size_t)(rb+r)*DIM + t] = fmaxf(acc[r]+bb, 0.f);
+  }
+}
+
+__global__ __launch_bounds__(256) void k_pack_pred(const void* Wsub, const void* Wobj, bf16* wpkP,
+                                                    const unsigned* flagp){
+  long idx = (long)blockIdx.x*256 + threadIdx.x;
+  long total = (long)2*PKS*PNT*512;
+  if (idx >= total) return;
+  int j = (int)(idx & 7), lane = (int)((idx>>3) & 63);
+  long rem = idx >> 9;
+  int ntile = (int)(rem % PNT); rem /= PNT;
+  int ks = (int)(rem % PKS); int page = (int)(rem / PKS);
+  int k = ks*32 + (lane>>4)*8 + j;
+  int n = ntile*16 + (lane&15);
+  const void* W = page ? Wobj : Wsub;
+  bool f32m = flagp[0] != 0u;
+  float v = 0.f;
+  if (k < 300) v = f32m ? ((const float*)W)[(size_t)k*NUME + n]
+                        : b2f(((const bf16*)W)[(size_t)k*NUME + n]);
+  wpkP[idx] = f2b(v);
+}
+
+__global__ __launch_bounds__(256) void k_prep_pred(const float* x4, const bf16* nSrel, const bf16* nOrel,
+                                                    const int* rel, bf16* Apack){
+  long idx = (long)blockIdx.x*256 + threadIdx.x;
+  if (idx >= (long)2*1024*320) return;
+  int j = (int)(idx % 320); long rem = idx/320;
+  int row = (int)(rem % 1024); int page = (int)(rem / 1024);
+  float v = 0.f;
+  if (j < 200) v = x4[((size_t)(page==0 ? 1024+row : row))*DIM + j];
+  else if (j < 300){
+    const bf16* re = (page==0) ? nOrel : nSrel;
+    v = b2f(re[(size_t)rel[row]*DIMR + (j-200)]);
+  }
+  Apack[idx] = f2b(v);
+}
+
+__global__ __launch_bounds__(256) void k_pred_mfma(const bf16* __restrict__ Apack, const bf16* __restrict__ wpkP,
+                                                   const bf16* bsub, const bf16* bobj, void* outb,
+                                                   const unsigned* flagp){
+  constexpr int SR = 320 + 8;
+  __shared__ bf16 As[64*SR];
+  int page = blockIdx.z;
+  int rb = blockIdx.y*64;
+  int cb = blockIdx.x*16;
+  int t = threadIdx.x;
+  const bf16* Ap = Apack + (size_t)page*1024*320;
+  for (int c=t; c<64*80; c+=256){
+    int m=c/80, j4=c%80;
+    *(uint2*)(As + m*SR + j4*4) = *(const uint2*)(Ap + (size_t)(rb+m)*320 + j4*4);
+  }
+  __syncthreads();
+  int lane = t&63, w = t>>6;
+  int n_idx = lane&15, quad = lane>>4;
+  const short8* wp8 = (const short8*)(wpkP + (size_t)page*PKS*PNT*512);
+  f32x4 acc[4][4];
+  #pragma unroll
+  for (int i=0;i<4;i++)
+    #pragma unroll
+    for (int mt=0;mt<4;mt++) acc[i][mt] = (f32x4){0.f,0.f,0.f,0.f};
+  short8 bz = {0,0,0,0,0,0,0,0};
+  for (int ks=0; ks<PKS; ks++){
+    short8 bfr[4];
+    #pragma unroll
+    for (int i=0;i<4;i++){
+      int ntile = cb + w + 4*i;
+      bfr[i] = (ntile < PNT) ? wp8[((size_t)ks*PNT + ntile)*64 + lane] : bz;
+    }
+    short8 afr[4];
+    #pragma unroll
+    for (int mt=0;mt<4;mt++) afr[mt] = *(const short8*)(As + (size_t)(mt*16 + n_idx)*SR + ks*32 + quad*8);
+    #pragma unroll
+    for (int i=0;i<4;i++)
+      #pragma unroll
+      for (int mt=0;mt<4;mt++)
+        acc[i][mt] = __builtin_amdgcn_mfma_f32_16x16x32_bf16(afr[mt], bfr[i], acc[i][mt], 0, 0, 0);
+  }
+  bool f32m = flagp[0] != 0u;
+  const bf16* bias = page ? bobj : bsub;
+  size_t elem_off = (size_t)page*BQ*NUME;
+  for (int i=0;i<4;i++){
+    int ntile = cb + w + 4*i;
+    if (ntile >= PNT) continue;
+    int n = ntile*16 + n_idx;
+    float bb = b2f(bias[n]);
+    #pragma unroll
+    for (int mt=0;mt<4;mt++){
+      #pragma unroll
+      for (int reg=0;reg<4;reg++){
+        int m = rb + mt*16 + quad*4 + reg;
+        size_t oi = elem_off + (size_t)m*NUME + n;
+        float val = acc[i][mt][reg] + bb;
+        if (f32m) ((float*)outb)[oi] = val; else ((bf16*)outb)[oi] = f2b(val);
+      }
+    }
   }
 }
 
@@ -679,37 +774,47 @@
   float* bgs1 = (float*)alloc(DIM*4);
   bf16* wpk0  = (bf16*)alloc((size_t)NET*4*13*512*2);
   bf16* wpk1  = (bf16*)alloc((size_t)NET*8*13*512*2);
+  bf16* wpkE0 = (bf16*)alloc((size_t)4*9*512*2);
+  bf16* wpkE1 = (bf16*)alloc((size_t)8*9*512*2);
   size_t arena = off;
-  bf16*  er0 = (bf16*)(base + arena);
-  bf16*  a0b = (bf16*)((char*)er0 + (size_t)NET*N1*8);
-  float* z0  = (float*)((char*)a0b + (size_t)NET*E0*8);
+  char* P1 = base + arena;
+  bf16*  a0b = (bf16*)P1;
+  float* z0  = (float*)(P1 + (size_t)NET*E0*8);
+  size_t ext1 = (size_t)NET*E0*8 + (size_t)NET*N1*16;
   char* A = base + arena;
-  bf16*  er1  = (bf16*)A;
-  bf16*  a1b  = (bf16*)(A + 1114112);
-  float* z1   = (float*)(A + 3290112);
-  float* msg1 = (float*)(A + 5518336);
-  float* hid  = (float*)(A + 12071936);
-  float* xln  = (float*)(A + 0);
-  float* x2   = (float*)(A + 6553600);
-  float* x3   = (float*)(A + 13107200);
-  float* x4   = (float*)(A + 19660800);
+  bf16*  a1b  = (bf16*)A;
+  float* z1   = (float*)(A + (size_t)NET*E1*8);
+  float* msg1 = (float*)(A + (size_t)NET*E1*8 + (size_t)NET*RNODES*16);
+  size_t msg1_off = (size_t)NET*E1*8 + (size_t)NET*RNODES*16;
+  float* hid  = (float*)(A + msg1_off + (size_t)RNODES*DIM*4);
+  size_t hid_off = msg1_off + (size_t)RNODES*DIM*4;
+  float* x3   = (float*)(A + hid_off + (size_t)NROWS*HD*4);
+  size_t x3_off = hid_off + (size_t)NROWS*HD*4;
+  float* x4   = (float*)(A + x3_off + (size_t)NROWS*HD*4);
+  size_t ext2 = x3_off + (size_t)NROWS*HD*4 + (size_t)NROWS*DIM*4;
   bf16* cWsubT = (bf16*)x0;
   bf16* cWobjT = (bf16*)((char*)x0 + (size_t)NUME*300*2);
 
-  size_t extent1 = (size_t)NET*N1*8 + (size_t)NET*E0*8 + (size_t)NET*N1*16;
-  size_t tail = (arena + extent1 + 255) & ~(size_t)255;
+  size_t extmax = ext1 > ext2 ? ext1 : ext2;
+  size_t tail = (arena + extmax + 255) & ~(size_t)255;
   size_t cntsz = (((size_t)(N1+1)*4) + 255) & ~(size_t)255;
   unsigned* cnt  = (unsigned*)(base + tail);
   unsigned* offs = (unsigned*)(base + tail + cntsz);
   unsigned* cur  = (unsigned*)(base + tail + 2*cntsz);
-  size_t ids_sz = (((size_t)NET*E0*4) + 255) & ~(size_t)255;
-  int* ids = (int*)(base + tail + 3*cntsz);
-  size_t F_off = tail + 3*cntsz + ids_sz;
+  size_t posar_sz = (((size_t)NET*E0*4) + 255) & ~(size_t)255;
+  int* posar = (int*)(base + tail + 3*cntsz);
+  size_t F_off = tail + 3*cntsz + posar_sz;
   bf16* fbuf = (bf16*)(base + F_off);
   size_t fcap = (ws_size > F_off) ? (ws_size - F_off) : 0;
   size_t relF0 = (size_t)E0*200*2, relF1 = (size_t)E1*200*2;
   int nrelc0 = (int)((fcap / relF0 < (size_t)NET) ? (fcap / relF0) : (size_t)NET);
   int nrelc1 = (int)((fcap / relF1 < (size_t)NET) ? (fcap / relF1) : (size_t)NET);
+  float* tab0 = (float*)fbuf;
+  float* tab1 = (float*)fbuf;
+  bool elrok0 = fcap >= (size_t)N0*TABW*4;
+  bool elrok1 = fcap >= (size_t)N1*TABW*4;
+  bf16* er0f = (bf16*)x1;
+  bf16* er1f = (bf16*)x0;
   size_t wpkP_sz = (size_t)2*PKS*PNT*512*2;
   size_t Apack_sz = (size_t)2*1024*320*2;
   bf16* wpkP  = (bf16*)(base + F_off);
@@ -740,11 +845,18 @@
   k_prep_w<<<GS(NET*DIN1*4),256,0,stream>>>(nWg1, nAl1, nAr1, wal1, war1, DIN1);
   k_pack<<<GS((long)NET*4*13*512),256,0,stream>>>(nWg0, wpk0, DIN0, 4);
   k_pack<<<GS((long)NET*8*13*512),256,0,stream>>>(nWg1, wpk1, DIN1, 8);
+  k_pack_walr<<<GS((long)4*9*512),256,0,stream>>>(wal0, war0, wpkE0, DIN0, 4);
+  k_pack_walr<<<GS((long)8*9*512),256,0,stream>>>(wal1, war1, wpkE1, DIN1, 8);
   k_bgs<<<GS(2*DIM),256,0,stream>>>(nBg0, nBg1, bgs0, bgs1);
   k_build_x0<<<GS((long)N0*DIN0),256,0,stream>>>(nid0, ts_p, nEmb, nTf, nTp, x0);
 
-  k_er<DIN0><<<GS((long)NET*N1),256,0,stream>>>(x0, war0, er0, N1);
-  k_edge<DIN0><<<GS((long)NET*E0),256,0,stream>>>(x0, wal0, er0, src0, dst0, a0b, z0, E0, N1);
+  if (elrok0){
+    k_elr<DIN0,4><<<dim3(N0/64),256,0,stream>>>(x0, wpkE0, tab0);
+    k_edge_lite<<<GS((long)NET*E0),256,0,stream>>>(tab0, src0, dst0, a0b, z0, E0, N1);
+  } else {
+    k_er<DIN0><<<GS((long)NET*N1),256,0,stream>>>(x0, war0, er0f, N1);
+    k_edge<DIN0><<<GS((long)NET*E0),256,0,stream>>>(x0, wal0, er0f, src0, dst0, a0b, z0, E0, N1);
+  }
   if (nrelc0 >= 1){
     for (int r0=0; r0<NET; r0+=nrelc0){
       int nr = (NET - r0 < nrelc0) ? (NET - r0) : nrelc0;
@@ -752,21 +864,26 @@
       k_fill_u32<<<GS((long)N1+1),256,0,stream>>>(cnt, 0u, (long)N1+1);
       k_count<<<GS(nEd),256,0,stream>>>(dst0 + (size_t)r0*E0, nEd, cnt);
       k_scan<<<dim3(1),256,0,stream>>>(cnt, offs, cur, N1);
-      k_fillcsr<<<GS(nEd),256,0,stream>>>(dst0 + (size_t)r0*E0, nEd, cur, ids);
-      k_acc_mfma<DIN0,4><<<dim3((E0+63)/64, nr),256,0,stream>>>(x0, wpk0, a0b, z0, src0, dst0,
+      k_fillcsr<<<GS(nEd),256,0,stream>>>(dst0 + (size_t)r0*E0, nEd, cur, posar);
+      k_acc_mfma<DIN0,4><<<dim3((E0+63)/64, nr),256,0,stream>>>(x0, wpk0, a0b, z0, src0, dst0, posar,
                                                                  msg0, fbuf, E0, N1, r0, 1);
-      k_gather<<<dim3((N1+3)/4),256,0,stream>>>(fbuf, offs, ids, msg0, N1, r0>0 ? 1 : 0);
+      k_gather_seq<<<dim3((N1+3)/4),256,0,stream>>>(fbuf, offs, msg0, N1, r0>0 ? 1 : 0);
     }
   } else {
     k_fill_u32<<<GS((long)N1*DIM),256,0,stream>>>((unsigned*)msg0, 0u, (long)N1*DIM);
-    k_acc_mfma<DIN0,4><<<dim3((E0+63)/64, NET),256,0,stream>>>(x0, wpk0, a0b, z0, src0, dst0,
+    k_acc_mfma<DIN0,4><<<dim3((E0+63)/64, NET),256,0,stream>>>(x0, wpk0, a0b, z0, src0, dst0, (int*)nullptr,
                                                                 msg0, (bf16*)nullptr, E0, N1, 0, 0);
   }
 
   k_build_x1<<<GS((long)N1*DIN1),256,0,stream>>>(nid0, ts_p, msg0, bgs0, nTf, nTp, x1);
   k_fill_u32<<<GS((long)NET*RNODES*4),256,0,stream>>>((unsigned*)z1, 0u, (long)NET*RNODES*4);
-  k_er<DIN1><<<GS((long)NET*RNODES),256,0,stream>>>(x1, war1, er1, RNODES);
-  k_edge<DIN1><<<GS((long)NET*E1),256,0,stream>>>(x1, wal1, er1, src1, dst1, a1b, z1, E1, RNODES);
+  if (elrok1){
+    k_elr<DIN1,8><<<dim3(N1/64),256,0,stream>>>(x1, wpkE1, tab1);
+    k_edge_lite<<<GS((long)NET*E1),256,0,stream>>>(tab1, src1, dst1, a1b, z1, E1, RNODES);
+  } else {
+    k_er<DIN1><<<GS((long)NET*RNODES),256,0,stream>>>(x1, war1, er1f, RNODES);
+    k_edge<DIN1><<<GS((long)NET*E1),256,0,stream>>>(x1, wal1, er1f, src1, dst1, a1b, z1, E1, RNODES);
+  }
   if (nrelc1 >= 1){
     for (int r0=0; r0<NET; r0+=nrelc1){
       int nr = (NET - r0 < nrelc1) ? (NET - r0) : nrelc1;
@@ -774,14 +891,14 @@
       k_fill_u32<<<GS((long)RNODES+1),256,0,stream>>>(cnt, 0u, (long)RNODES+1);
       k_count<<<GS(nEd),256,0,stream>>>(dst1 + (size_t)r0*E1, nEd, cnt);
       k_scan<<<dim3(1),256,0,stream>>>(cnt, offs, cur, RNODES);
-      k_fillcsr<<<GS(nEd),256,0,stream>>>(dst1 + (size_t)r0*E1, nEd, cur, ids);
-      k_acc_mfma<DIN1,8><<<dim3((E1+63)/64, nr),256,0,stream>>>(x1, wpk1, a1b, z1, src1, dst1,
+      k_fillcsr<<<GS(nEd),256,0,stream>>>(dst1 + (size_t)r0*E1, nEd, cur, posar);
+      k_acc_mfma<DIN1,8><<<dim3((E1+63)/64, nr),256,0,stream>>>(x1, wpk1, a1b, z1, src1, dst1, posar,
                                                                  msg1, fbuf, E1, RNODES, r0, 1);
-      k_gather<<<dim3((RNODES+3)/4),256,0,stream>>>(fbuf, offs, ids, msg1, RNODES, r0>0 ? 1 : 0);
+      k_gather_seq<<<dim3((RNODES+3)/4),256,0,stream>>>(fbuf, offs, msg1, RNODES, r0>0 ? 1 : 0);
     }
   } else {
     k_fill_u32<<<GS((long)RNODES*DIM),256,0,stream>>>((unsigned*)msg1, 0u, (long)RNODES*DIM);
-    k_acc_mfma<DIN1,8><<<dim3((E1+63)/64, NET),256,0,stream>>>(x1, wpk1, a1b, z1, src1, dst1,
+    k_acc_mfma<DIN1,8><<<dim3((E1+63)/64, NET),256,0,stream>>>(x1, wpk1, a1b, z1, src1, dst1, (int*)nullptr,
                                                                 msg1, (bf16*)nullptr, E1, RNODES, 0, 0);
   }
 
@@ -794,9 +911,7 @@
   k_scatter<<<dim3((KK+3)/4),256,0,stream>>>(copy_rows, copy_cols, rel, hid, nCsrel, nCorel,
                                              cWsubT, cWobjT, nCbsub, nCbobj, d_out, flagp);
 
-  k_ln<<<dim3(NROWS),256,0,stream>>>(hid, nLn0w, nLn0b, xln);
-  k_att<<<dim3(NROWS),256,0,stream>>>(xln, nWq, nBq, nWv, nBv, x2);
-  k_ln<<<dim3(NROWS),256,0,stream>>>(x2, nLn1w, nLn1b, x3);
+  k_att_ln<<<dim3(NROWS),256,0,stream>>>(hid, nLn0w, nLn0b, nWq, nBq, nWv, nBv, nLn1w, nLn1b, x3);
   k_d1<<<dim3(NROWS/8),256,0,stream>>>(x3, nWd1, nBd1, x4);
 
   if (predok){
```
